# Kernel optimization log

Measured on AMD Instinct MI355X. Metric: run time of the kernel, lower is better.

## Reference

```python
import jax, jax.numpy as jnp
import numpy as np

H = 512   # feature / hidden dim
T = 4     # bag_size (seq_len)
L = 4     # BiImprovedLSTM num_layers


def _ln(x, g, b, eps=1e-5):
    m = x.mean(-1, keepdims=True)
    v = ((x - m) ** 2).mean(-1, keepdims=True)
    return (x - m) / jnp.sqrt(v + eps) * g + b


def _graph_block(x, nodevec1, nodevec2, sc_w, sc_b, mp_w, mp_b, ec_w, ec_b,
                 gbl_w, gbl_b, gbln_g, gbln_b):
    # adaptive adjacency over the 512 feature-nodes
    adp = jax.nn.softmax(jax.nn.relu(nodevec1 @ nodevec2), axis=1)            # [512,512]
    h = jnp.transpose(x, (0, 2, 1))[:, None]                                  # [B,1,512,4]
    # start_conv is a 1x1 conv (d_model-c_out+1 == 1): 1 -> 32 channels
    h = h * sc_w.reshape(1, -1, 1, 1) + sc_b.reshape(1, -1, 1, 1)             # [B,32,512,4]
    # mixprop: add self loops, row-normalize, 1-step diffusion with alpha=0.7
    adj = adp + jnp.eye(adp.shape[0], dtype=x.dtype)
    a = adj / adj.sum(1, keepdims=True)
    hh = 0.7 * h + 0.3 * jnp.einsum('bcwl,vw->bcvl', h, a)                    # gdep=1
    ho = jnp.concatenate([h, hh], axis=1)                                     # [B,64,512,4]
    ho = jnp.einsum('bcvl,oc->bovl', ho, mp_w) + mp_b.reshape(1, -1, 1, 1)    # 1x1 mlp 64->32
    ho = jax.nn.gelu(ho, approximate=False)
    # end_conv: Conv2d(32 -> 4, kernel (1,4)) collapses the time axis
    oe = jnp.einsum('bcvl,ocl->bov', ho, ec_w) + ec_b.reshape(1, -1, 1)       # [B,4,512]
    g = oe @ gbl_w.T + gbl_b
    return _ln(x + g, gbln_g, gbln_b)


def _run_dir(W, Wb, U, Ub, xs, gws):
    # W,U: [L,5,H,H] (gate order i,f,o,c,s); xs,gws: [T,B,H]
    B = xs.shape[1]
    init = (jnp.zeros((L, B, H), xs.dtype), jnp.zeros((L, B, H), xs.dtype))
    def step(carry, inp):
        hs, cs = carry
        x_t, dw = inp
        nh, nc = [], []
        for l in range(L):
            z = (jnp.einsum('bi,goi->bgo', x_t, W[l]) + Wb[l]
                 + jnp.einsum('bi,goi->bgo', hs[l], U[l]) + Ub[l])            # [B,5,H]
            i_t = jax.nn.sigmoid(z[:, 0])
            f_t = jax.nn.sigmoid(z[:, 1])
            o_t = jax.nn.sigmoid(z[:, 2])
            ch  = jnp.tanh(z[:, 3])
            s_t = jax.nn.sigmoid(z[:, 4]) * dw
            c_t = f_t * cs[l] + i_t * ch * s_t
            h_t = o_t * jnp.tanh(c_t)
            nh.append(h_t); nc.append(c_t)
            x_t = h_t
        return (jnp.stack(nh), jnp.stack(nc)), x_t
    _, ys = jax.lax.scan(step, init, (xs, gws))
    return ys                                                                # [T,B,H]


def _mha(x, in_w, in_b, out_w, out_b, heads):
    B, N, E = x.shape
    qkv = x @ in_w.T + in_b
    q, k, v = jnp.split(qkv, 3, axis=-1)
    d = E // heads
    sh = lambda t: t.reshape(B, N, heads, d).transpose(0, 2, 1, 3)
    q, k, v = sh(q), sh(k), sh(v)
    attn = jax.nn.softmax(jnp.einsum('bhnd,bhmd->bhnm', q, k)
                          / jnp.sqrt(jnp.asarray(d, x.dtype)), axis=-1)
    o = jnp.einsum('bhnm,bhmd->bhnd', attn, v).transpose(0, 2, 1, 3).reshape(B, N, E)
    return o @ out_w.T + out_b


def _forward(x, nodevec1, nodevec2, sc_w, sc_b, mp_w, mp_b, ec_w, ec_b,
             gbl_w, gbl_b, gbln_g, gbln_b,
             lstm_W, lstm_Wb, lstm_U, lstm_Ub,
             mha_in_w, mha_in_b, mha_out_w, mha_out_b, ln1_g, ln1_b,
             qkv_w, dmin_g, dmin_b, pw_w, pw_b, fc_w, fc_b):
    xg = _graph_block(x, nodevec1, nodevec2, sc_w, sc_b, mp_w, mp_b,
                      ec_w, ec_b, gbl_w, gbl_b, gbln_g, gbln_b)              # [B,4,512]
    gw = jax.nn.softmax(xg, axis=-1)
    xs = jnp.transpose(xg, (1, 0, 2))
    gws = jnp.transpose(gw, (1, 0, 2))
    yf = _run_dir(lstm_W[0], lstm_Wb[0], lstm_U[0], lstm_Ub[0], xs, gws)
    yb = _run_dir(lstm_W[1], lstm_Wb[1], lstm_U[1], lstm_Ub[1],
                  xs[::-1], gws[::-1])[::-1]
    y = jnp.concatenate([yf, yb], axis=-1).transpose(1, 0, 2)                # [B,4,1024]
    y = _mha(y, mha_in_w, mha_in_b, mha_out_w, mha_out_b, 4)
    y = _ln(y, ln1_g, ln1_b)
    ori = y
    # MIL self-attention fusion: 8 heads, dim_head=128, no bias, no out proj
    B, N, E = y.shape
    qkv = y @ qkv_w.T
    q, k, v = jnp.split(qkv, 3, axis=-1)
    sh = lambda t: t.reshape(B, N, 8, 128).transpose(0, 2, 1, 3)
    q, k, v = sh(q), sh(k), sh(v)
    attn = jax.nn.softmax(jnp.einsum('bhnd,bhmd->bhnm', q, k) * (128 ** -0.5), axis=-1)
    z = jnp.einsum('bhnm,bhmd->bhnd', attn, v).transpose(0, 2, 1, 3).reshape(B, N, E)
    z = _ln(z, dmin_g, dmin_b)    # DMIN approximated as feature LayerNorm
    y = ori * jax.nn.sigmoid(z)                                               # [B,4,1024]
    # pwconv: Conv1d(4 -> 1, k=3, pad=1) over the bag axis
    x_fer = jax.lax.conv_general_dilated(y, pw_w, (1,), [(1, 1)],
                                         dimension_numbers=('NCH', 'OIH', 'NCH'))
    x_fer = x_fer[:, 0] + pw_b                                               # [B,1024]
    out = x_fer @ fc_w.T + fc_b                                              # [B,7]
    return out, x_fer


def setup_inputs() -> dict:
    key = jax.random.key(0)
    ks = jax.random.split(key, 16)
    B = 1024
    f32 = jnp.float32
    rn = lambda k, shape, s=0.02: (s * jax.random.normal(k, shape)).astype(f32)
    return {
        'x': jax.random.normal(ks[0], (B, T, H), f32),
        'nodevec1': jax.random.normal(ks[1], (H, 32), f32),
        'nodevec2': jax.random.normal(ks[2], (32, H), f32),
        'sc_w': rn(ks[3], (32,), 0.1), 'sc_b': jnp.zeros((32,), f32),
        'mp_w': rn(ks[4], (32, 64)), 'mp_b': jnp.zeros((32,), f32),
        'ec_w': rn(ks[5], (T, 32, T)), 'ec_b': jnp.zeros((T,), f32),
        'gbl_w': rn(ks[6], (H, H)), 'gbl_b': jnp.zeros((H,), f32),
        'gbln_g': jnp.ones((H,), f32), 'gbln_b': jnp.zeros((H,), f32),
        'lstm_W': rn(ks[7], (2, L, 5, H, H)), 'lstm_Wb': jnp.zeros((2, L, 5, H), f32),
        'lstm_U': rn(ks[8], (2, L, 5, H, H)), 'lstm_Ub': jnp.zeros((2, L, 5, H), f32),
        'mha_in_w': rn(ks[9], (3 * 2 * H, 2 * H)), 'mha_in_b': jnp.zeros((3 * 2 * H,), f32),
        'mha_out_w': rn(ks[10], (2 * H, 2 * H)), 'mha_out_b': jnp.zeros((2 * H,), f32),
        'ln1_g': jnp.ones((2 * H,), f32), 'ln1_b': jnp.zeros((2 * H,), f32),
        'qkv_w': rn(ks[11], (3 * 1024, 1024)),
        'dmin_g': jnp.ones((1024,), f32), 'dmin_b': jnp.zeros((1024,), f32),
        'pw_w': rn(ks[12], (1, T, 3), 0.1), 'pw_b': jnp.zeros((1,), f32),
        'fc_w': rn(ks[13], (7, 1024)), 'fc_b': jnp.zeros((7,), f32),
    }


def reference(x, nodevec1, nodevec2, sc_w, sc_b, mp_w, mp_b, ec_w, ec_b,
              gbl_w, gbl_b, gbln_g, gbln_b,
              lstm_W, lstm_Wb, lstm_U, lstm_Ub,
              mha_in_w, mha_in_b, mha_out_w, mha_out_b, ln1_g, ln1_b,
              qkv_w, dmin_g, dmin_b, pw_w, pw_b, fc_w, fc_b):
    return _forward(x, nodevec1, nodevec2, sc_w, sc_b, mp_w, mp_b, ec_w, ec_b,
                    gbl_w, gbl_b, gbln_g, gbln_b,
                    lstm_W, lstm_Wb, lstm_U, lstm_Ub,
                    mha_in_w, mha_in_b, mha_out_w, mha_out_b, ln1_g, ln1_b,
                    qkv_w, dmin_g, dmin_b, pw_w, pw_b, fc_w, fc_b)
```

## Files before the change

### kernel.cpp

```cpp
#include <hip/hip_runtime.h>

#define DEV __device__ __forceinline__

typedef __attribute__((ext_vector_type(8))) short bf16x8;
typedef __attribute__((ext_vector_type(8))) unsigned short u16x8;
typedef __attribute__((ext_vector_type(4))) float f32x4;

DEV unsigned short f2b(float f) {
  union { float f; unsigned u; } v;
  v.f = f;
  unsigned r = v.u + 0x7FFFu + ((v.u >> 16) & 1u);
  return (unsigned short)(r >> 16);
}
DEV float b2f(unsigned short u) {
  union { unsigned u; float f; } v;
  v.u = ((unsigned)u) << 16;
  return v.f;
}
DEV float sigmoidf(float x) { return 1.f / (1.f + expf(-x)); }

#define GL16(gp, lp)                                                        \
  __builtin_amdgcn_global_load_lds(                                         \
      (const __attribute__((address_space(1))) unsigned int*)(gp),          \
      (__attribute__((address_space(3))) unsigned int*)(lp), 16, 0, 0)

DEV float bsum(float v, float* red) {
#pragma unroll
  for (int off = 32; off; off >>= 1) v += __shfl_down(v, off, 64);
  int tid = threadIdx.x;
  __syncthreads();
  if ((tid & 63) == 0) red[tid >> 6] = v;
  __syncthreads();
  return red[0] + red[1] + red[2] + red[3];
}
DEV float bmax(float v, float* red) {
#pragma unroll
  for (int off = 32; off; off >>= 1) v = fmaxf(v, __shfl_down(v, off, 64));
  int tid = threadIdx.x;
  __syncthreads();
  if ((tid & 63) == 0) red[tid >> 6] = v;
  __syncthreads();
  return fmaxf(fmaxf(red[0], red[1]), fmaxf(red[2], red[3]));
}

__global__ __launch_bounds__(256) void k_cvt(const float* __restrict__ in,
                                             unsigned short* __restrict__ out) {
  long i = ((long)blockIdx.x * 256 + threadIdx.x) * 8;
  float4 a = *(const float4*)(in + i);
  float4 b = *(const float4*)(in + i + 4);
  u16x8 o;
  o[0] = f2b(a.x); o[1] = f2b(a.y); o[2] = f2b(a.z); o[3] = f2b(a.w);
  o[4] = f2b(b.x); o[5] = f2b(b.y); o[6] = f2b(b.z); o[7] = f2b(b.w);
  *(u16x8*)(out + i) = o;
}

__global__ __launch_bounds__(256) void k_adj(const float* __restrict__ nv1,
                                             const float* __restrict__ nv2,
                                             unsigned short* __restrict__ a) {
  const int v = blockIdx.x, tid = threadIdx.x;
  __shared__ float n1[32];
  __shared__ float red[4];
  if (tid < 32) n1[tid] = nv1[v * 32 + tid];
  __syncthreads();
  float r0, r1;
  {
    float s = 0.f;
#pragma unroll 8
    for (int k = 0; k < 32; ++k) s += n1[k] * nv2[k * 512 + tid];
    r0 = fmaxf(s, 0.f);
  }
  {
    float s = 0.f;
#pragma unroll 8
    for (int k = 0; k < 32; ++k) s += n1[k] * nv2[k * 512 + tid + 256];
    r1 = fmaxf(s, 0.f);
  }
  float mx = bmax(fmaxf(r0, r1), red);
  float e0 = expf(r0 - mx), e1 = expf(r1 - mx);
  float s = bsum(e0 + e1, red);
  float inv = 1.f / s;
  int w0 = tid, w1 = tid + 256;
  a[(long)v * 512 + w0] = f2b((e0 * inv + (w0 == v ? 1.f : 0.f)) * 0.5f);
  a[(long)v * 512 + w1] = f2b((e1 * inv + (w1 == v ? 1.f : 0.f)) * 0.5f);
}

__global__ void k_coef(const float* __restrict__ mp_w, const float* __restrict__ mp_b,
                       const float* __restrict__ sc_w, const float* __restrict__ sc_b,
                       float* __restrict__ cf) {
  int o = threadIdx.x;
  if (o < 32) {
    float A = 0.f, Bv = 0.f, Cv = 0.f;
    for (int cc = 0; cc < 32; ++cc) {
      float m1 = mp_w[o * 64 + cc], m2 = mp_w[o * 64 + 32 + cc];
      float sw = sc_w[cc], sb = sc_b[cc];
      A += (m1 + 0.7f * m2) * sw;
      Bv += 0.3f * m2 * sw;
      Cv += (m1 + m2) * sb;
    }
    cf[o] = A;
    cf[32 + o] = Bv;
    cf[64 + o] = Cv + mp_b[o];
  }
}

DEV void gemm_tile(const unsigned short* Ap, long lda, const unsigned short* Bp,
                   long ldb, int K, unsigned short* As, unsigned short* Bs,
                   int bm, int bn, int tid, f32x4 (&acc)[4][4]) {
  const int lane = tid & 63, wave = tid >> 6;
  const int wr = wave >> 1, wc = wave & 1;
  const int lr = lane & 15, lg = lane >> 4;
  const int sg = tid >> 3, sc8 = (tid & 7) * 8;
  const unsigned short* Arow = Ap + (long)(bm * 128 + sg) * lda + sc8;
  const unsigned short* Brow = Bp + (long)(bn * 128 + sg) * ldb + sc8;
  for (int k0 = 0; k0 < K; k0 += 64) {
    __syncthreads();
#pragma unroll
    for (int i = 0; i < 4; ++i) {
      GL16(Arow + (long)(i * 32) * lda + k0, &As[i * 2048 + wave * 512]);
      GL16(Brow + (long)(i * 32) * ldb + k0, &Bs[i * 2048 + wave * 512]);
    }
    __syncthreads();
#pragma unroll
    for (int kk = 0; kk < 2; ++kk) {
      bf16x8 af[4], bq[4];
#pragma unroll
      for (int m = 0; m < 4; ++m)
        af[m] = *(const bf16x8*)&As[(wr * 64 + m * 16 + lr) * 64 + kk * 32 + lg * 8];
#pragma unroll
      for (int n = 0; n < 4; ++n)
        bq[n] = *(const bf16x8*)&Bs[(wc * 64 + n * 16 + lr) * 64 + kk * 32 + lg * 8];
#pragma unroll
      for (int m = 0; m < 4; ++m)
#pragma unroll
        for (int n = 0; n < 4; ++n)
          acc[m][n] = __builtin_amdgcn_mfma_f32_16x16x32_bf16(af[m], bq[n],
                                                              acc[m][n], 0, 0, 0);
    }
  }
}

__global__ __launch_bounds__(256) void k_bgemm(
    const unsigned short* __restrict__ A, long lda,
    const unsigned short* __restrict__ B, long ldb,
    const float* __restrict__ bias, float* __restrict__ C, long ldc, int K) {
  __shared__ unsigned short As[8192], Bs[8192];
  f32x4 acc[4][4];
#pragma unroll
  for (int m = 0; m < 4; ++m)
#pragma unroll
    for (int n = 0; n < 4; ++n) acc[m][n] = (f32x4){0.f, 0.f, 0.f, 0.f};
  gemm_tile(A, lda, B, ldb, K, As, Bs, blockIdx.x, blockIdx.y, threadIdx.x, acc);
  const int lane = threadIdx.x & 63, wave = threadIdx.x >> 6;
  const int wr = wave >> 1, wc = wave & 1, lr = lane & 15, lg = lane >> 4;
  const long crow0 = (long)blockIdx.x * 128 + wr * 64;
  const int col0 = blockIdx.y * 128 + wc * 64;
#pragma unroll
  for (int n = 0; n < 4; ++n) {
    const int col = col0 + n * 16 + lr;
    const float bv = bias ? bias[col] : 0.f;
#pragma unroll
    for (int m = 0; m < 4; ++m) {
      const long rbase = (crow0 + m * 16 + lg * 4) * ldc + col;
#pragma unroll
      for (int j = 0; j < 4; ++j) C[rbase + (long)j * ldc] = acc[m][n][j] + bv;
    }
  }
}

struct LStage {
  const unsigned short* a0[6];
  const unsigned short* a2[6];
  const unsigned short* w[6];
  const unsigned short* u[6];
  unsigned short* zo[6];
  long lda0[6];
};

__global__ __launch_bounds__(256) void k_lgemm(LStage p) {
  __shared__ unsigned short As[8192], Bs[8192];
  const int z = blockIdx.z;
  f32x4 acc[4][4];
#pragma unroll
  for (int m = 0; m < 4; ++m)
#pragma unroll
    for (int n = 0; n < 4; ++n) acc[m][n] = (f32x4){0.f, 0.f, 0.f, 0.f};
  gemm_tile(p.a0[z], p.lda0[z], p.w[z], 512, 512, As, Bs, blockIdx.x,
            blockIdx.y, threadIdx.x, acc);
  gemm_tile(p.a2[z], 512, p.u[z], 512, 512, As, Bs, blockIdx.x, blockIdx.y,
            threadIdx.x, acc);
  unsigned short* zo = p.zo[z];
  const int lane = threadIdx.x & 63, wave = threadIdx.x >> 6;
  const int wr = wave >> 1, wc = wave & 1, lr = lane & 15, lg = lane >> 4;
  const long crow0 = (long)blockIdx.x * 128 + wr * 64;
  const int col0 = blockIdx.y * 128 + wc * 64;
#pragma unroll
  for (int n = 0; n < 4; ++n) {
    const int col = col0 + n * 16 + lr;
#pragma unroll
    for (int m = 0; m < 4; ++m) {
      const long rbase = (crow0 + m * 16 + lg * 4) * 2560 + col;
#pragma unroll
      for (int j = 0; j < 4; ++j) zo[rbase + (long)j * 2560] = f2b(acc[m][n][j]);
    }
  }
}

struct GStage {
  const unsigned short* z[6];
  int tt[6];
  int ll[6];
};

__global__ __launch_bounds__(256) void k_gates(
    GStage g, const float* __restrict__ Wb, const float* __restrict__ Ub,
    const unsigned short* __restrict__ gwbf, unsigned short* __restrict__ hbf,
    float* __restrict__ c, unsigned short* __restrict__ ylbf) {
  const int s = blockIdx.y, dir = s & 1;
  const int t = g.tt[s], l = g.ll[s];
  const unsigned short* zp = g.z[s];
  const int idx = blockIdx.x * 256 + threadIdx.x;
  const int b = idx >> 9, o = idx & 511;
  const long boff = (long)(dir * 4 + l) * 2560 + o;
  const long zb = (long)b * 2560 + o;
  float zi = b2f(zp[zb]) + Wb[boff] + Ub[boff];
  float zf = b2f(zp[zb + 512]) + Wb[boff + 512] + Ub[boff + 512];
  float zoo = b2f(zp[zb + 1024]) + Wb[boff + 1024] + Ub[boff + 1024];
  float zc = b2f(zp[zb + 1536]) + Wb[boff + 1536] + Ub[boff + 1536];
  float zs = b2f(zp[zb + 2048]) + Wb[boff + 2048] + Ub[boff + 2048];
  const int tok = dir ? 3 - t : t;
  float dw = b2f(gwbf[(long)b * 2048 + tok * 512 + o]);
  const long hc = ((long)(dir * 4 + l) * 1024 + b) * 512 + o;
  float i_t = sigmoidf(zi), f_t = sigmoidf(zf), o_t = sigmoidf(zoo);
  float ch = tanhf(zc);
  float s_t = sigmoidf(zs) * dw;
  float cn = f_t * c[hc] + i_t * ch * s_t;
  float hn = o_t * tanhf(cn);
  c[hc] = cn;
  hbf[hc] = f2b(hn);
  if (l == 3) ylbf[(long)b * 4096 + tok * 1024 + dir * 512 + o] = f2b(hn);
}

__global__ __launch_bounds__(256) void k_oe(const float* __restrict__ x,
                                            const float* __restrict__ yg,
                                            const float* __restrict__ cf,
                                            const float* __restrict__ ec_w,
                                            const float* __restrict__ ec_b,
                                            unsigned short* __restrict__ oe) {
  const int b = blockIdx.x;
  const int v = blockIdx.y * 256 + threadIdx.x;
  __shared__ float ecs[512];
  __shared__ float cfs[96];
  __shared__ float ebs[4];
  if (threadIdx.x < 96) cfs[threadIdx.x] = cf[threadIdx.x];
  if (threadIdx.x < 4) ebs[threadIdx.x] = ec_b[threadIdx.x];
  for (int i = threadIdx.x; i < 512; i += 256) ecs[i] = ec_w[i];
  __syncthreads();
  float xl[4], yl[4];
#pragma unroll
  for (int l = 0; l < 4; ++l) {
    long off = ((long)b * 4 + l) * 512 + v;
    xl[l] = x[off];
    yl[l] = yg[off];
  }
  float o0 = ebs[0], o1 = ebs[1], o2 = ebs[2], o3 = ebs[3];
  for (int cc = 0; cc < 32; ++cc) {
    float A = cfs[cc], Bv = cfs[32 + cc], Cv = cfs[64 + cc];
#pragma unroll
    for (int l = 0; l < 4; ++l) {
      float u = fmaf(A, xl[l], fmaf(Bv, yl[l], Cv));
      float gu = 0.5f * u * (1.f + erff(u * 0.70710678118654752f));
      o0 = fmaf(ecs[(0 * 32 + cc) * 4 + l], gu, o0);
      o1 = fmaf(ecs[(1 * 32 + cc) * 4 + l], gu, o1);
      o2 = fmaf(ecs[(2 * 32 + cc) * 4 + l], gu, o2);
      o3 = fmaf(ecs[(3 * 32 + cc) * 4 + l], gu, o3);
    }
  }
  oe[((long)b * 4 + 0) * 512 + v] = f2b(o0);
  oe[((long)b * 4 + 1) * 512 + v] = f2b(o1);
  oe[((long)b * 4 + 2) * 512 + v] = f2b(o2);
  oe[((long)b * 4 + 3) * 512 + v] = f2b(o3);
}

__global__ __launch_bounds__(256) void k_lngw(const float* __restrict__ x,
                                              const float* __restrict__ g,
                                              const float* __restrict__ gg,
                                              const float* __restrict__ gb,
                                              unsigned short* __restrict__ xg,
                                              unsigned short* __restrict__ gw) {
  const long r = blockIdx.x;
  const int tid = threadIdx.x;
  __shared__ float red[4];
  const float* xp = x + r * 512;
  const float* gp = g + r * 512;
  float a0 = xp[tid] + gp[tid];
  float a1 = xp[tid + 256] + gp[tid + 256];
  float m = bsum(a0 + a1, red) * (1.f / 512.f);
  float q = (a0 - m) * (a0 - m) + (a1 - m) * (a1 - m);
  float var = bsum(q, red) * (1.f / 512.f);
  float rstd = rsqrtf(var + 1e-5f);
  float v0 = (a0 - m) * rstd * gg[tid] + gb[tid];
  float v1 = (a1 - m) * rstd * gg[tid + 256] + gb[tid + 256];
  xg[r * 512 + tid] = f2b(v0);
  xg[r * 512 + tid + 256] = f2b(v1);
  float mx = bmax(fmaxf(v0, v1), red);
  float e0 = expf(v0 - mx), e1 = expf(v1 - mx);
  float s = bsum(e0 + e1, red);
  float inv = 1.f / s;
  gw[r * 512 + tid] = f2b(e0 * inv);
  gw[r * 512 + tid + 256] = f2b(e1 * inv);
}

__global__ __launch_bounds__(256) void k_attn(const float* __restrict__ qkv,
                                              unsigned short* __restrict__ outb,
                                              float* __restrict__ outf, int d,
                                              float scale, int obf) {
  const int b = blockIdx.x, h = blockIdx.y;
  __shared__ float qs[4][256], ks[4][256], vs[4][256];
  __shared__ float sc[4][4];
  const int tid = threadIdx.x;
  for (int tok = 0; tok < 4; ++tok) {
    const float* base = qkv + ((long)b * 4 + tok) * 3072 + h * d;
    for (int j = tid; j < d; j += 256) {
      qs[tok][j] = base[j];
      ks[tok][j] = base[1024 + j];
      vs[tok][j] = base[2048 + j];
    }
  }
  __syncthreads();
  if (tid < 16) {
    int i = tid >> 2, j = tid & 3;
    float s = 0.f;
    for (int dd = 0; dd < d; ++dd) s += qs[i][dd] * ks[j][dd];
    sc[i][j] = s * scale;
  }
  __syncthreads();
  if (tid < 4) {
    float m = fmaxf(fmaxf(sc[tid][0], sc[tid][1]), fmaxf(sc[tid][2], sc[tid][3]));
    float e0 = expf(sc[tid][0] - m), e1 = expf(sc[tid][1] - m);
    float e2 = expf(sc[tid][2] - m), e3 = expf(sc[tid][3] - m);
    float inv = 1.f / (e0 + e1 + e2 + e3);
    sc[tid][0] = e0 * inv;
    sc[tid][1] = e1 * inv;
    sc[tid][2] = e2 * inv;
    sc[tid][3] = e3 * inv;
  }
  __syncthreads();
  for (int idx = tid; idx < 4 * d; idx += 256) {
    int i = idx / d, dd = idx - i * d;
    float o = sc[i][0] * vs[0][dd] + sc[i][1] * vs[1][dd] + sc[i][2] * vs[2][dd] +
              sc[i][3] * vs[3][dd];
    long off = ((long)b * 4 + i) * 1024 + (long)h * d + dd;
    if (obf) outb[off] = f2b(o);
    else outf[off] = o;
  }
}

__global__ __launch_bounds__(256) void k_ln1024(const float* __restrict__ in,
                                                const float* __restrict__ gg,
                                                const float* __restrict__ bb,
                                                float* __restrict__ outf,
                                                unsigned short* __restrict__ outb) {
  const long r = blockIdx.x;
  const int tid = threadIdx.x;
  __shared__ float red[4];
  const float* ip = in + r * 1024;
  float v[4];
#pragma unroll
  for (int i = 0; i < 4; ++i) v[i] = ip[tid + i * 256];
  float m = bsum(v[0] + v[1] + v[2] + v[3], red) * (1.f / 1024.f);
  float q = 0.f;
#pragma unroll
  for (int i = 0; i < 4; ++i) q += (v[i] - m) * (v[i] - m);
  float rstd = rsqrtf(bsum(q, red) * (1.f / 1024.f) + 1e-5f);
#pragma unroll
  for (int i = 0; i < 4; ++i) {
    int cidx = tid + i * 256;
    float o = (v[i] - m) * rstd * gg[cidx] + bb[cidx];
    outf[r * 1024 + cidx] = o;
    outb[r * 1024 + cidx] = f2b(o);
  }
}

__global__ __launch_bounds__(256) void k_dmin(const float* __restrict__ zin,
                                              const float* __restrict__ ori,
                                              const float* __restrict__ gg,
                                              const float* __restrict__ bb,
                                              float* __restrict__ y2) {
  const long r = blockIdx.x;
  const int tid = threadIdx.x;
  __shared__ float red[4];
  const float* ip = zin + r * 1024;
  float v[4];
#pragma unroll
  for (int i = 0; i < 4; ++i) v[i] = ip[tid + i * 256];
  float m = bsum(v[0] + v[1] + v[2] + v[3], red) * (1.f / 1024.f);
  float q = 0.f;
#pragma unroll
  for (int i = 0; i < 4; ++i) q += (v[i] - m) * (v[i] - m);
  float rstd = rsqrtf(bsum(q, red) * (1.f / 1024.f) + 1e-5f);
#pragma unroll
  for (int i = 0; i < 4; ++i) {
    int cidx = tid + i * 256;
    float ln = (v[i] - m) * rstd * gg[cidx] + bb[cidx];
    y2[r * 1024 + cidx] = ori[r * 1024 + cidx] * (1.f / (1.f + expf(-ln)));
  }
}

__global__ __launch_bounds__(256) void k_pw(const float* __restrict__ y2,
                                            const float* __restrict__ pw,
                                            const float* __restrict__ pb,
                                            float* __restrict__ xfer) {
  const int b = blockIdx.x;
  __shared__ float w[12];
  if (threadIdx.x < 12) w[threadIdx.x] = pw[threadIdx.x];
  __syncthreads();
  const float bias = pb[0];
  for (int e = threadIdx.x; e < 1024; e += 256) {
    float acc = bias;
#pragma unroll
    for (int c = 0; c < 4; ++c) {
      const float* yr = y2 + (long)b * 4096 + (long)c * 1024;
      if (e > 0) acc = fmaf(yr[e - 1], w[c * 3 + 0], acc);
      acc = fmaf(yr[e], w[c * 3 + 1], acc);
      if (e < 1023) acc = fmaf(yr[e + 1], w[c * 3 + 2], acc);
    }
    xfer[(long)b * 1024 + e] = acc;
  }
}

__global__ __launch_bounds__(256) void k_fc(const float* __restrict__ xf,
                                            const float* __restrict__ fw,
                                            const float* __restrict__ fb,
                                            float* __restrict__ out) {
  const int b = blockIdx.x, tid = threadIdx.x;
  float acc[7] = {0.f, 0.f, 0.f, 0.f, 0.f, 0.f, 0.f};
  for (int e = tid; e < 1024; e += 256) {
    float xv = xf[(long)b * 1024 + e];
#pragma unroll
    for (int j = 0; j < 7; ++j) acc[j] = fmaf(xv, fw[j * 1024 + e], acc[j]);
  }
  __shared__ float red[4][7];
#pragma unroll
  for (int j = 0; j < 7; ++j) {
    float v = acc[j];
#pragma unroll
    for (int off = 32; off; off >>= 1) v += __shfl_down(v, off, 64);
    if ((tid & 63) == 0) red[tid >> 6][j] = v;
  }
  __syncthreads();
  if (tid < 7)
    out[(long)b * 7 + tid] =
        red[0][tid] + red[1][tid] + red[2][tid] + red[3][tid] + fb[tid];
}

static const int ST[8][3][2] = {
    {{0, 0}, {0, 0}, {0, 0}},
    {{1, 0}, {0, 1}, {0, 0}},
    {{2, 0}, {1, 1}, {0, 2}},
    {{1, 2}, {0, 3}, {0, 0}},
    {{3, 0}, {2, 1}, {0, 0}},
    {{3, 1}, {2, 2}, {1, 3}},
    {{3, 2}, {2, 3}, {0, 0}},
    {{3, 3}, {0, 0}, {0, 0}},
};
static const int NC[8] = {1, 2, 3, 2, 2, 3, 2, 1};

extern "C" void kernel_launch(void* const* d_in, const int* in_sizes, int n_in,
                              void* d_out, int out_size, void* d_ws,
                              size_t ws_size, hipStream_t stream) {
  const float* x = (const float*)d_in[0];
  const float* nv1 = (const float*)d_in[1];
  const float* nv2 = (const float*)d_in[2];
  const float* sc_w = (const float*)d_in[3];
  const float* sc_b = (const float*)d_in[4];
  const float* mp_w = (const float*)d_in[5];
  const float* mp_b = (const float*)d_in[6];
  const float* ec_w = (const float*)d_in[7];
  const float* ec_b = (const float*)d_in[8];
  const float* gbl_w = (const float*)d_in[9];
  const float* gbl_b = (const float*)d_in[10];
  const float* gbln_g = (const float*)d_in[11];
  const float* gbln_b = (const float*)d_in[12];
  const float* lstm_W = (const float*)d_in[13];
  const float* lstm_Wb = (const float*)d_in[14];
  const float* lstm_U = (const float*)d_in[15];
  const float* lstm_Ub = (const float*)d_in[16];
  const float* mha_in_w = (const float*)d_in[17];
  const float* mha_in_b = (const float*)d_in[18];
  const float* mha_out_w = (const float*)d_in[19];
  const float* mha_out_b = (const float*)d_in[20];
  const float* ln1_g = (const float*)d_in[21];
  const float* ln1_b = (const float*)d_in[22];
  const float* qkv_w = (const float*)d_in[23];
  const float* dmin_g = (const float*)d_in[24];
  const float* dmin_b = (const float*)d_in[25];
  const float* pw_w = (const float*)d_in[26];
  const float* pw_b = (const float*)d_in[27];
  const float* fc_w = (const float*)d_in[28];
  const float* fc_b = (const float*)d_in[29];

  char* wsb = (char*)d_ws;
  float* out = (float*)d_out;
  float* xfer = out + 1024 * 7;

  unsigned short* xgbf = (unsigned short*)(wsb + 0);
  unsigned short* gwbf = (unsigned short*)(wsb + 4194304);
  unsigned short* Wbf = (unsigned short*)(wsb + 8388608);
  unsigned short* Ubf = (unsigned short*)(wsb + 29360128);
  unsigned short* hbf = (unsigned short*)(wsb + 50331648);
  float* cst = (float*)(wsb + 58720256);
  unsigned short* zbf = (unsigned short*)(wsb + 75497472);
  unsigned short* ylbf = (unsigned short*)(wsb + 106954752);
  unsigned short* xbf = (unsigned short*)(wsb + 75497472);
  unsigned short* aBf = (unsigned short*)(wsb + 79691776);
  unsigned short* gblbf = (unsigned short*)(wsb + 80216064);
  float* wY = (float*)(wsb + 80740352);
  unsigned short* oebf = (unsigned short*)(wsb + 89128960);
  float* wCF = (float*)(wsb + 93323264);
  unsigned short* m1w = (unsigned short*)(wsb + 0);
  float* qkv = (float*)(wsb + 6291456);
  unsigned short* attb = (unsigned short*)(wsb + 56623104);
  float* attf = (float*)(wsb + 56623104);
  unsigned short* m2w = (unsigned short*)(wsb + 73400320);
  float* mhay = (float*)(wsb + 75497472);
  float* orif = (float*)(wsb + 92274688);
  unsigned short* orib = (unsigned short*)(wsb + 109051904);
  unsigned short* qw2 = (unsigned short*)(wsb + 0);
  float* y2 = (float*)(wsb + 75497472);

  hipMemsetAsync(wsb + 50331648, 0, 25165824, stream);

  k_cvt<<<1024, 256, 0, stream>>>(x, xbf);
  k_cvt<<<5120, 256, 0, stream>>>(lstm_W, Wbf);
  k_cvt<<<5120, 256, 0, stream>>>(lstm_U, Ubf);
  k_cvt<<<128, 256, 0, stream>>>(gbl_w, gblbf);

  k_adj<<<512, 256, 0, stream>>>(nv1, nv2, aBf);
  k_coef<<<1, 64, 0, stream>>>(mp_w, mp_b, sc_w, sc_b, wCF);
  k_bgemm<<<dim3(32, 4), 256, 0, stream>>>(xbf, 512, aBf, 512, nullptr, wY,
                                           512, 512);
  k_oe<<<dim3(1024, 2), 256, 0, stream>>>(x, wY, wCF, ec_w, ec_b, oebf);
  k_bgemm<<<dim3(32, 4), 256, 0, stream>>>(oebf, 512, gblbf, 512, gbl_b, wY,
                                           512, 512);
  k_lngw<<<4096, 256, 0, stream>>>(x, wY, gbln_g, gbln_b, xgbf, gwbf);

  for (int s = 0; s < 8; ++s) {
    const int nc = NC[s];
    LStage lp;
    GStage gp;
    for (int ci = 0; ci < nc; ++ci) {
      const int t = ST[s][ci][0], l = ST[s][ci][1];
      for (int dir = 0; dir < 2; ++dir) {
        const int sl = ci * 2 + dir;
        if (l == 0) {
          lp.a0[sl] = xgbf + (dir ? (3 - t) : t) * 512;
          lp.lda0[sl] = 2048;
        } else {
          lp.a0[sl] = hbf + (long)(dir * 4 + l - 1) * 524288;
          lp.lda0[sl] = 512;
        }
        lp.a2[sl] = hbf + (long)(dir * 4 + l) * 524288;
        lp.w[sl] = Wbf + (long)(dir * 4 + l) * 1310720;
        lp.u[sl] = Ubf + (long)(dir * 4 + l) * 1310720;
        unsigned short* zslice = zbf + (long)ci * 5242880 + (long)dir * 2621440;
        lp.zo[sl] = zslice;
        gp.z[sl] = zslice;
        gp.tt[sl] = t;
        gp.ll[sl] = l;
      }
    }
    k_lgemm<<<dim3(8, 20, nc * 2), 256, 0, stream>>>(lp);
    k_gates<<<dim3(2048, nc * 2), 256, 0, stream>>>(gp, lstm_Wb, lstm_Ub, gwbf,
                                                    hbf, cst, ylbf);
  }

  k_cvt<<<1536, 256, 0, stream>>>(mha_in_w, m1w);
  k_bgemm<<<dim3(32, 24), 256, 0, stream>>>(ylbf, 1024, m1w, 1024, mha_in_b,
                                            qkv, 3072, 1024);
  k_attn<<<dim3(1024, 4), 256, 0, stream>>>(qkv, attb, nullptr, 256, 1.f / 16.f, 1);
  k_cvt<<<512, 256, 0, stream>>>(mha_out_w, m2w);
  k_bgemm<<<dim3(32, 8), 256, 0, stream>>>(attb, 1024, m2w, 1024, mha_out_b,
                                           mhay, 1024, 1024);
  k_ln1024<<<4096, 256, 0, stream>>>(mhay, ln1_g, ln1_b, orif, orib);

  k_cvt<<<1536, 256, 0, stream>>>(qkv_w, qw2);
  k_bgemm<<<dim3(32, 24), 256, 0, stream>>>(orib, 1024, qw2, 1024, nullptr,
                                            qkv, 3072, 1024);
  k_attn<<<dim3(1024, 8), 256, 0, stream>>>(qkv, nullptr, attf, 128,
                                            0.08838834764831845f, 0);
  k_dmin<<<4096, 256, 0, stream>>>(attf, orif, dmin_g, dmin_b, y2);

  k_pw<<<1024, 256, 0, stream>>>(y2, pw_w, pw_b, xfer);
  k_fc<<<1024, 256, 0, stream>>>(xfer, fc_w, fc_b, out);
}
```

Baseline: 933.2 us.

## Double-buffer LDS tiles in GEMM and fuse LSTM W/U segments into one pipeline

Replaces the single-buffered GEMM tile loop, which synced twice per 64-wide K step, with a double-buffered loop over 32-wide K steps. The next tile is prefetched with global_load_lds while MFMAs run on the current one, and MFMA issue priority is raised. The LSTM gate GEMM now streams its W and U K-segments through one continuous pipeline instead of two separate tile loops. This hides global load latency behind compute at the cost of more barriers per K and a smaller K slice per stage.

```diff
diff --git a/kernel.cpp b/kernel.cpp
--- a/kernel.cpp
+++ b/kernel.cpp
@@ -103,39 +103,63 @@
   }
 }
 
-DEV void gemm_tile(const unsigned short* Ap, long lda, const unsigned short* Bp,
-                   long ldb, int K, unsigned short* As, unsigned short* Bs,
-                   int bm, int bn, int tid, f32x4 (&acc)[4][4]) {
+DEV void gemm_pipe(const unsigned short* A0, long lda0,
+                   const unsigned short* B0, long ldb0,
+                   const unsigned short* A1, long lda1,
+                   const unsigned short* B1, long ldb1,
+                   int sps, int dual, int bm, int bn, int tid,
+                   unsigned short* lds, f32x4 (&acc)[4][4]) {
   const int lane = tid & 63, wave = tid >> 6;
   const int wr = wave >> 1, wc = wave & 1;
   const int lr = lane & 15, lg = lane >> 4;
-  const int sg = tid >> 3, sc8 = (tid & 7) * 8;
-  const unsigned short* Arow = Ap + (long)(bm * 128 + sg) * lda + sc8;
-  const unsigned short* Brow = Bp + (long)(bn * 128 + sg) * ldb + sc8;
-  for (int k0 = 0; k0 < K; k0 += 64) {
-    __syncthreads();
-#pragma unroll
-    for (int i = 0; i < 4; ++i) {
-      GL16(Arow + (long)(i * 32) * lda + k0, &As[i * 2048 + wave * 512]);
-      GL16(Brow + (long)(i * 32) * ldb + k0, &Bs[i * 2048 + wave * 512]);
-    }
-    __syncthreads();
-#pragma unroll
-    for (int kk = 0; kk < 2; ++kk) {
-      bf16x8 af[4], bq[4];
-#pragma unroll
-      for (int m = 0; m < 4; ++m)
-        af[m] = *(const bf16x8*)&As[(wr * 64 + m * 16 + lr) * 64 + kk * 32 + lg * 8];
+  const int srow = wave * 16 + (lane >> 2);
+  const int scx = (lane & 3) * 8;
+  const unsigned short* pa0 = A0 + (long)(bm * 128 + srow) * lda0 + scx;
+  const unsigned short* pa1 = A1 + (long)(bm * 128 + srow) * lda1 + scx;
+  const unsigned short* pb0 = B0 + (long)(bn * 128 + srow) * ldb0 + scx;
+  const unsigned short* pb1 = B1 + (long)(bn * 128 + srow) * ldb1 + scx;
+  const int aoff = (wr * 64 + lr) * 32 + lg * 8;
+  const int boff = 4096 + (wc * 64 + lr) * 32 + lg * 8;
+  const int tot = dual ? sps * 2 : sps;
+
+  auto stage = [&](int t, int buf) {
+    const int seg = (dual && t >= sps) ? 1 : 0;
+    const long k0 = (long)(t - seg * sps) * 32;
+    const unsigned short* ap = (seg ? pa1 : pa0) + k0;
+    const unsigned short* bp = (seg ? pb1 : pb0) + k0;
+    const long la = seg ? lda1 : lda0;
+    const long lb = seg ? ldb1 : ldb0;
+    unsigned short* d = lds + buf * 8192;
+    GL16(ap, d + wave * 512);
+    GL16(ap + 64 * la, d + 2048 + wave * 512);
+    GL16(bp, d + 4096 + wave * 512);
+    GL16(bp + 64 * lb, d + 6144 + wave * 512);
+  };
+
+  stage(0, 0);
+  asm volatile("s_waitcnt vmcnt(0)" ::: "memory");
+  __builtin_amdgcn_s_barrier();
+  int cur = 0;
+  for (int t = 0; t < tot; ++t) {
+    if (t + 1 < tot) stage(t + 1, cur ^ 1);
+    const unsigned short* base = lds + cur * 8192;
+    bf16x8 af[4], bq[4];
+#pragma unroll
+    for (int m = 0; m < 4; ++m) af[m] = *(const bf16x8*)&base[aoff + m * 512];
+#pragma unroll
+    for (int n = 0; n < 4; ++n) bq[n] = *(const bf16x8*)&base[boff + n * 512];
+    __builtin_amdgcn_s_setprio(1);
+#pragma unroll
+    for (int m = 0; m < 4; ++m)
 #pragma unroll
       for (int n = 0; n < 4; ++n)
-        bq[n] = *(const bf16x8*)&Bs[(wc * 64 + n * 16 + lr) * 64 + kk * 32 + lg * 8];
-#pragma unroll
-      for (int m = 0; m < 4; ++m)
-#pragma unroll
-        for (int n = 0; n < 4; ++n)
-          acc[m][n] = __builtin_amdgcn_mfma_f32_16x16x32_bf16(af[m], bq[n],
-                                                              acc[m][n], 0, 0, 0);
-    }
+        acc[m][n] = __builtin_amdgcn_mfma_f32_16x16x32_bf16(af[m], bq[n],
+                                                            acc[m][n], 0, 0, 0);
+    __builtin_amdgcn_s_setprio(0);
+    asm volatile("s_waitcnt vmcnt(0)" ::: "memory");
+    __builtin_amdgcn_sched_barrier(0);
+    __builtin_amdgcn_s_barrier();
+    cur ^= 1;
   }
 }
 
@@ -143,13 +167,14 @@
     const unsigned short* __restrict__ A, long lda,
     const unsigned short* __restrict__ B, long ldb,
     const float* __restrict__ bias, float* __restrict__ C, long ldc, int K) {
-  __shared__ unsigned short As[8192], Bs[8192];
+  __shared__ unsigned short lds[16384];
   f32x4 acc[4][4];
 #pragma unroll
   for (int m = 0; m < 4; ++m)
 #pragma unroll
     for (int n = 0; n < 4; ++n) acc[m][n] = (f32x4){0.f, 0.f, 0.f, 0.f};
-  gemm_tile(A, lda, B, ldb, K, As, Bs, blockIdx.x, blockIdx.y, threadIdx.x, acc);
+  gemm_pipe(A, lda, B, ldb, A, lda, B, ldb, K / 32, 0, blockIdx.x, blockIdx.y,
+            threadIdx.x, lds, acc);
   const int lane = threadIdx.x & 63, wave = threadIdx.x >> 6;
   const int wr = wave >> 1, wc = wave & 1, lr = lane & 15, lg = lane >> 4;
   const long crow0 = (long)blockIdx.x * 128 + wr * 64;
@@ -177,17 +202,15 @@
 };
 
 __global__ __launch_bounds__(256) void k_lgemm(LStage p) {
-  __shared__ unsigned short As[8192], Bs[8192];
+  __shared__ unsigned short lds[16384];
   const int z = blockIdx.z;
   f32x4 acc[4][4];
 #pragma unroll
   for (int m = 0; m < 4; ++m)
 #pragma unroll
     for (int n = 0; n < 4; ++n) acc[m][n] = (f32x4){0.f, 0.f, 0.f, 0.f};
-  gemm_tile(p.a0[z], p.lda0[z], p.w[z], 512, 512, As, Bs, blockIdx.x,
-            blockIdx.y, threadIdx.x, acc);
-  gemm_tile(p.a2[z], 512, p.u[z], 512, 512, As, Bs, blockIdx.x, blockIdx.y,
-            threadIdx.x, acc);
+  gemm_pipe(p.a0[z], p.lda0[z], p.w[z], 512, p.a2[z], 512, p.u[z], 512, 16, 1,
+            blockIdx.x, blockIdx.y, threadIdx.x, lds, acc);
   unsigned short* zo = p.zo[z];
   const int lane = threadIdx.x & 63, wave = threadIdx.x >> 6;
   const int wr = wave >> 1, wc = wave & 1, lr = lane & 15, lg = lane >> 4;
```

Result: faster. 859.6 us (-7.9%).
